# Optimization experiments

Hardware: AMD Instinct MI355X
Metric: run time of the kernel (lower is better)

The kernel has to match this reference:

```python
import jax, jax.numpy as jnp
import numpy as np

FS = 128; WIN = 4; C_IN = 64; C_OUT = 512; BATCH = 1024
K = FS // 4            # conv kernel = 32
STRIDE = K // 2        # 16
WS = FS * WIN          # 512 samples
T = (WS - K) // STRIDE + 1  # 31 time steps
THRESH = 1.0
BN_EPS = 1e-5

# snntorch-style spike with ATan surrogate (alpha=2): fwd Heaviside, bwd 1/(1+(pi*x)^2)
@jax.custom_vjp
def spike_fn(x):
    return (x > 0).astype(x.dtype)

def _spike_fwd(x):
    return (x > 0).astype(x.dtype), x

def _spike_bwd(x, g):
    return (g / (1.0 + (jnp.pi * x) ** 2),)

spike_fn.defvjp(_spike_fwd, _spike_bwd)

def leaky_step(inp, mem, beta):
    # snntorch Leaky, reset_mechanism='subtract': reset computed from PREVIOUS mem, detached
    reset = jax.lax.stop_gradient((mem > THRESH).astype(mem.dtype))
    mem_new = jnp.clip(beta, 0.0, 1.0) * mem + inp - reset * THRESH
    spk = spike_fn(mem_new - THRESH)
    return spk, mem_new

def setup_inputs() -> dict:
    key = jax.random.key(0)
    ks = jax.random.split(key, 10)
    return {
        "x": jax.random.normal(ks[0], (BATCH, C_IN, WS), jnp.float32),
        "conv_w": jax.random.normal(ks[1], (C_OUT, C_IN, K), jnp.float32) * (1.0 / np.sqrt(C_IN * K)),
        "conv_b": jax.random.normal(ks[2], (C_OUT,), jnp.float32) * 0.01,
        "bn_gamma": jnp.ones((C_OUT,), jnp.float32),
        "bn_beta": jnp.zeros((C_OUT,), jnp.float32),
        "bn_mean": jnp.zeros((C_OUT,), jnp.float32),
        "bn_var": jnp.ones((C_OUT,), jnp.float32),
        "fc1_w": jax.random.normal(ks[3], (C_OUT, C_OUT), jnp.float32) * (1.0 / np.sqrt(C_OUT)),
        "fc1_b": jax.random.normal(ks[4], (C_OUT,), jnp.float32) * 0.01,
        "fc2_w": jax.random.normal(ks[5], (2, C_OUT), jnp.float32) * (1.0 / np.sqrt(C_OUT)),
        "fc2_b": jax.random.normal(ks[6], (2,), jnp.float32) * 0.01,
        "beta_enc": jax.random.uniform(ks[7], (C_OUT,), jnp.float32),
        "beta_hid": jax.random.uniform(ks[8], (C_OUT,), jnp.float32),
        "beta_out": jax.random.uniform(ks[9], (2,), jnp.float32),
    }

def reference(x, conv_w, conv_b, bn_gamma, bn_beta, bn_mean, bn_var,
              fc1_w, fc1_b, fc2_w, fc2_b, beta_enc, beta_hid, beta_out):
    # Conv1d: x [B, C_in, WS] -> [B, C_out, T]
    out = jax.lax.conv_general_dilated(
        x, conv_w, window_strides=(STRIDE,), padding='VALID',
        dimension_numbers=('NCH', 'OIH', 'NCH')) + conv_b[None, :, None]
    # BatchNorm1d (eval mode with running stats); dropout is identity in eval
    inv = jax.lax.rsqrt(bn_var + BN_EPS)
    out = bn_gamma[None, :, None] * (out - bn_mean[None, :, None]) * inv[None, :, None] + bn_beta[None, :, None]
    seq = jnp.transpose(out, (2, 0, 1))  # [T, B, C_out]

    mems0 = (jnp.zeros((BATCH, C_OUT), out.dtype),
             jnp.zeros((BATCH, C_OUT), out.dtype),
             jnp.zeros((BATCH, 2), out.dtype))

    def step(carry, xt):
        em, hm, om = carry
        spk_e, em = leaky_step(xt, em, beta_enc)
        cur1 = spk_e @ fc1_w.T + fc1_b
        spk_h, hm = leaky_step(cur1, hm, beta_hid)
        cur2 = spk_h @ fc2_w.T + fc2_b
        spk_o, om = leaky_step(cur2, om, beta_out)
        return (em, hm, om), (spk_o, om)

    (em, hm, om), (spk_rec, mem_rec) = jax.lax.scan(step, mems0, seq)
    return om, spk_rec, mem_rec
```

## Files before the change

kernel.cpp:

```cpp
#include <hip/hip_runtime.h>

#define T_STEPS 31
#define CIN     64
#define COUT    512
#define WSLEN   512
#define CSTRIDE 16
#define KRED    2048
#define NBATCH  1024
#define BCHUNK  512
#define MCHUNK  (BCHUNK * T_STEPS)
#define NMT     (MCHUNK / 16)

typedef int v4i __attribute__((ext_vector_type(4)));

__device__ __forceinline__ double clip01d(double v) { return fmin(fmax(v, 0.0), 1.0); }

__device__ __forceinline__ void gl_lds16(const void* g, void* l) {
    __builtin_amdgcn_global_load_lds(
        (const __attribute__((address_space(1))) void*)g,
        (__attribute__((address_space(3))) void*)l, 16, 0, 0);
}

__device__ __forceinline__ void dig5(float4 f, unsigned int w[5]) {
    float vv[4] = {f.x, f.y, f.z, f.w};
    unsigned int w0 = 0, w1 = 0, w2 = 0, w3 = 0, w4 = 0;
    #pragma unroll
    for (int e = 0; e < 4; ++e) {
        float v  = vv[e];
        float c0 = rintf(v * 16384.0f);
        float r1 = fmaf(c0, -6.103515625e-05f, v);
        float c1 = rintf(r1 * 268435456.0f);
        float r2 = fmaf(c1, -3.725290298461914e-09f, r1);
        float c2 = rintf(r2 * 34359738368.0f);
        int i0 = (int)c0, i1 = (int)c1, i2 = (int)c2;
        int d2 = ((i0 + 64) & 127) - 64;
        int d1 = (i0 - d2) >> 7;
        int d4 = ((i1 + 64) & 127) - 64;
        int d3 = (i1 - d4) >> 7;
        w0 |= (unsigned int)(d1 & 255) << (8 * e);
        w1 |= (unsigned int)(d2 & 255) << (8 * e);
        w2 |= (unsigned int)(d3 & 255) << (8 * e);
        w3 |= (unsigned int)(d4 & 255) << (8 * e);
        w4 |= (unsigned int)(i2 & 255) << (8 * e);
    }
    w[0] = w0; w[1] = w1; w[2] = w2; w[3] = w3; w[4] = w4;
}

__global__ __launch_bounds__(256) void prep_fc1_kernel(
    const float* __restrict__ fc1_w, float* __restrict__ fc1wT)
{
    int idx = blockIdx.x * 256 + threadIdx.x;
    int co = idx & 511;
    int r  = idx >> 9;
    fc1wT[idx] = fc1_w[co * COUT + r];
}

__global__ __launch_bounds__(256) void prep_bd_kernel(
    const float* __restrict__ conv_w, signed char* __restrict__ Bd)
{
    int t  = blockIdx.x * 256 + threadIdx.x;
    int k4 = (t & 511) << 2;
    int co = t >> 9;
    float4 w4 = *(const float4*)(conv_w + (size_t)co * KRED + k4);
    float4 v4 = make_float4(w4.x * 4.0f, w4.y * 4.0f, w4.z * 4.0f, w4.w * 4.0f);
    unsigned int pk[5];
    dig5(v4, pk);
    int off = (((k4 >> 6) * 32 + (co >> 4)) << 10)
            + ((co & 15) + ((k4 >> 4) & 3) * 16) * 16 + (k4 & 15);
    #pragma unroll
    for (int q = 0; q < 5; ++q)
        *(unsigned int*)(Bd + q * 1048576 + off) = pk[q];
}

__global__ __launch_bounds__(256) void prep_fd_kernel(
    const float* __restrict__ fc1_w, signed char* __restrict__ Fd)
{
    int t  = blockIdx.x * 256 + threadIdx.x;
    int k4 = (t & 127) << 2;
    int co = t >> 7;
    float4 w4 = *(const float4*)(fc1_w + (size_t)co * COUT + k4);
    float4 v4 = make_float4(w4.x * 4.0f, w4.y * 4.0f, w4.z * 4.0f, w4.w * 4.0f);
    unsigned int pk[5];
    dig5(v4, pk);
    int off = (((k4 >> 6) * 32 + (co >> 4)) << 10)
            + ((co & 15) + ((k4 >> 4) & 3) * 16) * 16 + (k4 & 15);
    #pragma unroll
    for (int q = 0; q < 5; ++q)
        *(unsigned int*)(Fd + q * 262144 + off) = pk[q];
}

__global__ __launch_bounds__(512) void conv_bn_i8v6_kernel(
    const float* __restrict__ x, const signed char* __restrict__ Bd,
    const float* __restrict__ conv_b,
    const float* __restrict__ bn_gamma, const float* __restrict__ bn_beta,
    const float* __restrict__ bn_mean,  const float* __restrict__ bn_var,
    double* __restrict__ seq, int b_base)
{
    __shared__ __align__(16) signed char Alds[5 * 2048];
    __shared__ __align__(16) signed char Blds[5 * 8192];

    const int tid = threadIdx.x;
    const int nMB = MCHUNK / 32;
    const int bm  = blockIdx.x % nMB;
    const int bnk = blockIdx.x / nMB;
    const int m0 = bm * 32, n0 = bnk * 128;

    const int rA  = tid & 31;
    const int gA  = tid >> 5;
    const int kqA = gA & 3;
    const int jq  = gA >> 2;
    const int mA  = m0 + rA;
    const int bA  = b_base + mA / T_STEPS;
    const int tA  = mA % T_STEPS;
    const float* xp = x + (size_t)bA * CIN * WSLEN + tA * CSTRIDE;
    const int awb  = ((rA >> 4) << 10) + ((rA & 15) + kqA * 16) * 16 + jq * 4;
    const int kloc = kqA * 16 + jq * 4;

    const int wv  = tid >> 6;
    const int l   = tid & 63;
    const int rgM = wv >> 2;
    const int cw  = wv & 3;

    v4i acc[2][5];
    #pragma unroll
    for (int s = 0; s < 2; ++s)
        #pragma unroll
        for (int d = 0; d < 5; ++d) acc[s][d] = (v4i){0, 0, 0, 0};

    float4 sxa = *(const float4*)(xp + (kloc >> 5) * WSLEN + (kloc & 31));

    for (int kt = 0; kt < 32; ++kt) {
        unsigned int pa[5];
        dig5(make_float4(sxa.x * 0.125f, sxa.y * 0.125f, sxa.z * 0.125f, sxa.w * 0.125f), pa);

        __syncthreads();
        #pragma unroll
        for (int p = 0; p < 5; ++p)
            *(unsigned int*)(Alds + p * 2048 + awb) = pa[p];

        #pragma unroll
        for (int i = 0; i < 5; ++i) {
            const int s   = wv * 5 + i;
            const int q   = s >> 3;
            const int ctl = s & 7;
            const signed char* gsrc = Bd + (size_t)q * 1048576
                + (((size_t)(kt * 32 + bnk * 8 + ctl)) << 10) + l * 16;
            gl_lds16(gsrc, Blds + q * 8192 + ctl * 1024);
        }

        if (kt + 1 < 32) {
            int gk = (kt + 1) * 64 + kloc;
            sxa = *(const float4*)(xp + (gk >> 5) * WSLEN + (gk & 31));
        }
        __syncthreads();

        v4i aF[5];
        #pragma unroll
        for (int p = 0; p < 5; ++p)
            aF[p] = *(const v4i*)(Alds + p * 2048 + (rgM << 10) + (l << 4));

        #define MF(A_, B_, C_) __builtin_amdgcn_mfma_i32_16x16x64_i8(A_, B_, C_, 0, 0, 0)
        #pragma unroll
        for (int s = 0; s < 2; ++s) {
            const signed char* bb = Blds + ((cw * 2 + s) << 10) + (l << 4);
            v4i b0 = *(const v4i*)(bb);
            v4i b1 = *(const v4i*)(bb + 8192);
            v4i b2 = *(const v4i*)(bb + 16384);
            v4i b3 = *(const v4i*)(bb + 24576);
            v4i b4 = *(const v4i*)(bb + 32768);
            acc[s][0] = MF(aF[0], b0, acc[s][0]);
            acc[s][1] = MF(aF[1], b0, MF(aF[0], b1, acc[s][1]));
            acc[s][2] = MF(aF[2], b0, MF(aF[1], b1, MF(aF[0], b2, acc[s][2])));
            acc[s][3] = MF(aF[3], b0, MF(aF[2], b1, MF(aF[1], b2, MF(aF[0], b3, acc[s][3]))));
            acc[s][4] = MF(aF[4], b0, MF(aF[3], b1, MF(aF[2], b2, MF(aF[1], b3, MF(aF[0], b4, acc[s][4])))));
        }
        #undef MF
    }

    const int l15 = l & 15;
    const int rq  = l >> 4;
    #pragma unroll
    for (int s = 0; s < 2; ++s) {
        const int co = n0 + (cw * 2 + s) * 16 + l15;
        const double g   = (double)bn_gamma[co];
        const double be  = (double)bn_beta[co];
        const double mn  = (double)bn_mean[co];
        const double vr  = (double)bn_var[co];
        const double cb  = (double)conv_b[co];
        const double inv = 1.0 / sqrt(vr + 1e-5);
        #pragma unroll
        for (int r = 0; r < 4; ++r) {
            double v = (double)acc[s][0][r] * 0x1p-13
                     + (double)acc[s][1][r] * 0x1p-20
                     + (double)acc[s][2][r] * 0x1p-27
                     + (double)acc[s][3][r] * 0x1p-34
                     + (double)acc[s][4][r] * 0x1p-41;
            int m = m0 + rgM * 16 + rq * 4 + r;
            seq[(size_t)m * COUT + co] = g * (v + cb - mn) * inv + be;
        }
    }
}

__global__ __launch_bounds__(512) void enc_scan_kernel(
    const double* __restrict__ seq, const float* __restrict__ beta_enc,
    signed char* __restrict__ Sd)
{
    const int c = threadIdx.x;
    const int b = blockIdx.x;
    const double be = clip01d((double)beta_enc[c]);
    const double* sp = seq + (size_t)b * T_STEPS * COUT + c;
    const size_t cblk = (size_t)(c >> 6) * NMT;
    const int    coff = ((c >> 4) & 3) * 16;
    const int    j    = c & 15;
    double em = 0.0;
    for (int t = 0; t < T_STEPS; ++t) {
        double e = be * em + sp[(size_t)t * COUT] - ((em > 1.0) ? 1.0 : 0.0);
        em = e;
        int m = b * T_STEPS + t;
        Sd[((cblk + (m >> 4)) << 10) + ((m & 15) + coff) * 16 + j] =
            (e > 1.0) ? (signed char)1 : (signed char)0;
    }
}

__global__ __launch_bounds__(512) void fc1_gemm_kernel(
    const signed char* __restrict__ Sd, const signed char* __restrict__ Fd,
    double* __restrict__ cur1)
{
    __shared__ __align__(16) signed char AldsK[2048];
    __shared__ __align__(16) signed char BldsK[5 * 8192];

    const int tid = threadIdx.x;
    const int nMB = MCHUNK / 32;
    const int bm  = blockIdx.x % nMB;
    const int bnk = blockIdx.x / nMB;
    const int m0 = bm * 32, n0 = bnk * 128;

    const int wv  = tid >> 6;
    const int l   = tid & 63;
    const int rgM = wv >> 2;
    const int cw  = wv & 3;

    v4i acc[2][5];
    #pragma unroll
    for (int s = 0; s < 2; ++s)
        #pragma unroll
        for (int d = 0; d < 5; ++d) acc[s][d] = (v4i){0, 0, 0, 0};

    for (int kt = 0; kt < 8; ++kt) {
        __syncthreads();
        #pragma unroll
        for (int i = 0; i < 5; ++i) {
            const int s   = wv * 5 + i;
            const int q   = s >> 3;
            const int ctl = s & 7;
            const signed char* gsrc = Fd + (size_t)q * 262144
                + (((size_t)(kt * 32 + bnk * 8 + ctl)) << 10) + l * 16;
            gl_lds16(gsrc, BldsK + q * 8192 + ctl * 1024);
        }
        if (wv < 2) {
            const signed char* gsrc = Sd
                + (((size_t)(kt * NMT + bm * 2 + wv)) << 10) + l * 16;
            gl_lds16(gsrc, AldsK + wv * 1024);
        }
        __syncthreads();

        v4i aF = *(const v4i*)(AldsK + (rgM << 10) + (l << 4));
        #define MF(A_, B_, C_) __builtin_amdgcn_mfma_i32_16x16x64_i8(A_, B_, C_, 0, 0, 0)
        #pragma unroll
        for (int s = 0; s < 2; ++s) {
            const signed char* bb = BldsK + ((cw * 2 + s) << 10) + (l << 4);
            acc[s][0] = MF(aF, *(const v4i*)(bb),         acc[s][0]);
            acc[s][1] = MF(aF, *(const v4i*)(bb + 8192),  acc[s][1]);
            acc[s][2] = MF(aF, *(const v4i*)(bb + 16384), acc[s][2]);
            acc[s][3] = MF(aF, *(const v4i*)(bb + 24576), acc[s][3]);
            acc[s][4] = MF(aF, *(const v4i*)(bb + 32768), acc[s][4]);
        }
        #undef MF
    }

    const int l15 = l & 15;
    const int rq  = l >> 4;
    #pragma unroll
    for (int s = 0; s < 2; ++s) {
        const int co = n0 + (cw * 2 + s) * 16 + l15;
        #pragma unroll
        for (int r = 0; r < 4; ++r) {
            double v = (double)acc[s][0][r] * 0x1p-9
                     + (double)acc[s][1][r] * 0x1p-16
                     + (double)acc[s][2][r] * 0x1p-23
                     + (double)acc[s][3][r] * 0x1p-30
                     + (double)acc[s][4][r] * 0x1p-37;
            int m = m0 + rgM * 16 + rq * 4 + r;
            cur1[(size_t)m * COUT + co] = v;
        }
    }
}

__global__ __launch_bounds__(512, 4) void hid_out_scan_kernel(
    const double* __restrict__ cur1, const float* __restrict__ fc1_b,
    const float* __restrict__ fc2_w, const float* __restrict__ fc2_b,
    const float* __restrict__ beta_hid, const float* __restrict__ beta_out,
    float* __restrict__ out, int b_base)
{
    __shared__ double red[8][2];

    const int tid  = threadIdx.x;
    const int lane = tid & 63;
    const int wave = tid >> 6;
    const int row  = blockIdx.x;
    const int brow = b_base + row;

    const double bh  = clip01d((double)beta_hid[tid]);
    const double f1b = (double)fc1_b[tid];
    const double w2a = (double)fc2_w[tid];
    const double w2b = (double)fc2_w[COUT + tid];

    double bo = 0.0, f2b = 0.0, om = 0.0;
    if (tid < 2) { bo = clip01d((double)beta_out[tid]); f2b = (double)fc2_b[tid]; }

    double hm = 0.0;
    const double* cp = cur1 + (size_t)row * T_STEPS * COUT + tid;

    for (int t = 0; t < T_STEPS; ++t) {
        double cur = cp[(size_t)t * COUT] + f1b;
        double h = bh * hm + cur - ((hm > 1.0) ? 1.0 : 0.0);
        hm = h;
        double sh = (h > 1.0) ? 1.0 : 0.0;
        double p0 = sh * w2a;
        double p1 = sh * w2b;
        #pragma unroll
        for (int off = 32; off > 0; off >>= 1) {
            p0 += __shfl_down(p0, off);
            p1 += __shfl_down(p1, off);
        }
        if (lane == 0) { red[wave][0] = p0; red[wave][1] = p1; }
        __syncthreads();
        if (tid < 2) {
            double cur2 = f2b;
            #pragma unroll
            for (int w = 0; w < 8; ++w) cur2 += red[w][tid];
            double o = bo * om + cur2 - ((om > 1.0) ? 1.0 : 0.0);
            om = o;
            float so = (o > 1.0) ? 1.0f : 0.0f;
            int bidx = brow * 2 + tid;
            out[2048 + t * 2048 + bidx] = so;
            out[2048 + 63488 + t * 2048 + bidx] = (float)o;
            if (t == T_STEPS - 1) out[bidx] = (float)o;
        }
        __syncthreads();
    }
}

__global__ __launch_bounds__(512, 4) void snn_scan_v3_kernel(
    const double* __restrict__ seq, const float* __restrict__ fc1wT,
    const float* __restrict__ fc1_b, const float* __restrict__ fc2_w,
    const float* __restrict__ fc2_b, const float* __restrict__ beta_enc,
    const float* __restrict__ beta_hid, const float* __restrict__ beta_out,
    float* __restrict__ out, int b_base)
{
    __shared__ int   list[COUT];
    __shared__ int   wcnt[8];
    __shared__ double red[8][2];

    const int tid  = threadIdx.x;
    const int lane = tid & 63;
    const int wave = tid >> 6;
    const int row  = blockIdx.x;
    const int brow = b_base + row;

    const double be  = clip01d((double)beta_enc[tid]);
    const double bh  = clip01d((double)beta_hid[tid]);
    const double f1b = (double)fc1_b[tid];
    const double w2a = (double)fc2_w[tid];
    const double w2b = (double)fc2_w[COUT + tid];

    double bo = 0.0, f2b = 0.0, om = 0.0;
    if (tid < 2) { bo = clip01d((double)beta_out[tid]); f2b = (double)fc2_b[tid]; }

    double em = 0.0, hm = 0.0;
    const double* sp = seq + (size_t)row * T_STEPS * COUT + tid;

    for (int t = 0; t < T_STEPS; ++t) {
        double inp = sp[(size_t)t * COUT];
        double e = be * em + inp - ((em > 1.0) ? 1.0 : 0.0);
        em = e;
        bool spike = (e > 1.0);

        unsigned long long mask = __ballot(spike);
        if (lane == 0) wcnt[wave] = __popcll(mask);
        __syncthreads();

        int base = 0, cnt = 0;
        #pragma unroll
        for (int w = 0; w < 8; ++w) {
            int v = wcnt[w];
            base += (w < wave) ? v : 0;
            cnt  += v;
        }
        if (spike) {
            int pos = base + __popcll(mask & ((1ull << lane) - 1ull));
            list[pos] = tid;
        }
        __syncthreads();

        double s0 = 0.0, s1 = 0.0, s2 = 0.0, s3 = 0.0;
        const float* fw = fc1wT + tid;
        int i = 0;
        for (; i + 4 <= cnt; i += 4) {
            int cA = list[i], cB = list[i + 1], cC = list[i + 2], cD = list[i + 3];
            s0 += (double)fw[(size_t)cA * COUT];
            s1 += (double)fw[(size_t)cB * COUT];
            s2 += (double)fw[(size_t)cC * COUT];
            s3 += (double)fw[(size_t)cD * COUT];
        }
        for (; i < cnt; ++i) s0 += (double)fw[(size_t)list[i] * COUT];
        double cur1 = ((s0 + s1) + (s2 + s3)) + f1b;

        double h = bh * hm + cur1 - ((hm > 1.0) ? 1.0 : 0.0);
        hm = h;
        double sh = (h > 1.0) ? 1.0 : 0.0;
        double p0 = sh * w2a;
        double p1 = sh * w2b;
        #pragma unroll
        for (int off = 32; off > 0; off >>= 1) {
            p0 += __shfl_down(p0, off);
            p1 += __shfl_down(p1, off);
        }
        if (lane == 0) { red[wave][0] = p0; red[wave][1] = p1; }
        __syncthreads();

        if (tid < 2) {
            double cur2 = f2b;
            #pragma unroll
            for (int w = 0; w < 8; ++w) cur2 += red[w][tid];
            double o = bo * om + cur2 - ((om > 1.0) ? 1.0 : 0.0);
            om = o;
            float so = (o > 1.0) ? 1.0f : 0.0f;
            int bidx = brow * 2 + tid;
            out[2048 + t * 2048 + bidx] = so;
            out[2048 + 63488 + t * 2048 + bidx] = (float)o;
            if (t == T_STEPS - 1) out[bidx] = (float)o;
        }
    }
}

extern "C" void kernel_launch(void* const* d_in, const int* in_sizes, int n_in,
                              void* d_out, int out_size, void* d_ws, size_t ws_size,
                              hipStream_t stream)
{
    const float* x        = (const float*)d_in[0];
    const float* conv_w   = (const float*)d_in[1];
    const float* conv_b   = (const float*)d_in[2];
    const float* bn_gamma = (const float*)d_in[3];
    const float* bn_beta  = (const float*)d_in[4];
    const float* bn_mean  = (const float*)d_in[5];
    const float* bn_var   = (const float*)d_in[6];
    const float* fc1_w    = (const float*)d_in[7];
    const float* fc1_b    = (const float*)d_in[8];
    const float* fc2_w    = (const float*)d_in[9];
    const float* fc2_b    = (const float*)d_in[10];
    const float* beta_enc = (const float*)d_in[11];
    const float* beta_hid = (const float*)d_in[12];
    const float* beta_out = (const float*)d_in[13];
    float* out = (float*)d_out;

    const size_t NEED_BIG = 16ull * 1048576 + (size_t)MCHUNK * COUT * 8;
    signed char* Bd = (signed char*)d_ws;

    if (ws_size >= NEED_BIG) {
        signed char* Fd  = (signed char*)d_ws + 5 * 1048576;
        signed char* Sd  = (signed char*)d_ws + 7 * 1048576;
        double*      seq = (double*)((char*)d_ws + 16 * 1048576);

        prep_bd_kernel<<<1024, 256, 0, stream>>>(conv_w, Bd);
        prep_fd_kernel<<<256, 256, 0, stream>>>(fc1_w, Fd);

        for (int chunk = 0; chunk < 2; ++chunk) {
            int b_base = chunk * BCHUNK;
            conv_bn_i8v6_kernel<<<(MCHUNK / 32) * (COUT / 128), 512, 0, stream>>>(
                x, Bd, conv_b, bn_gamma, bn_beta, bn_mean, bn_var, seq, b_base);
            enc_scan_kernel<<<BCHUNK, 512, 0, stream>>>(seq, beta_enc, Sd);
            fc1_gemm_kernel<<<(MCHUNK / 32) * (COUT / 128), 512, 0, stream>>>(
                Sd, Fd, seq);
            hid_out_scan_kernel<<<BCHUNK, 512, 0, stream>>>(
                seq, fc1_b, fc2_w, fc2_b, beta_hid, beta_out, out, b_base);
        }
    } else {
        float*  fc1wT = (float*)((char*)d_ws + 5 * 1048576);
        double* seq   = (double*)((char*)d_ws + 6 * 1048576);

        prep_bd_kernel<<<1024, 256, 0, stream>>>(conv_w, Bd);
        prep_fc1_kernel<<<1024, 256, 0, stream>>>(fc1_w, fc1wT);

        for (int chunk = 0; chunk < 2; ++chunk) {
            int b_base = chunk * BCHUNK;
            conv_bn_i8v6_kernel<<<(MCHUNK / 32) * (COUT / 128), 512, 0, stream>>>(
                x, Bd, conv_b, bn_gamma, bn_beta, bn_mean, bn_var, seq, b_base);
            snn_scan_v3_kernel<<<BCHUNK, 512, 0, stream>>>(
                seq, fc1wT, fc1_b, fc2_w, fc2_b, beta_enc, beta_hid, beta_out, out, b_base);
        }
    }
}
```

Before: 712.4 us.

## Double-buffer conv GEMM LDS tiles and halve N tile per block

The conv+BN int8 MFMA kernel now double-buffers its A and B tiles in LDS. The next k-step's global-to-LDS loads and input digit splitting overlap the current step's MFMAs, so the loop needs one barrier per iteration instead of two. The N tile per block shrinks from 128 to 64 output channels, which doubles the grid size and halves per-wave accumulators. In exchange, each block has fewer MFMAs per barrier and the conv weights are loaded twice as often overall.

```diff
diff --git a/kernel.cpp b/kernel.cpp
--- a/kernel.cpp
+++ b/kernel.cpp
@@ -89,21 +89,21 @@
         *(unsigned int*)(Fd + q * 262144 + off) = pk[q];
 }
 
-__global__ __launch_bounds__(512) void conv_bn_i8v6_kernel(
+__global__ __launch_bounds__(512) void conv_bn_i8v8_kernel(
     const float* __restrict__ x, const signed char* __restrict__ Bd,
     const float* __restrict__ conv_b,
     const float* __restrict__ bn_gamma, const float* __restrict__ bn_beta,
     const float* __restrict__ bn_mean,  const float* __restrict__ bn_var,
     double* __restrict__ seq, int b_base)
 {
-    __shared__ __align__(16) signed char Alds[5 * 2048];
-    __shared__ __align__(16) signed char Blds[5 * 8192];
+    __shared__ __align__(16) signed char Abuf[2][5 * 2048];
+    __shared__ __align__(16) signed char Bbuf[2][5 * 4096];
 
     const int tid = threadIdx.x;
     const int nMB = MCHUNK / 32;
     const int bm  = blockIdx.x % nMB;
     const int bnk = blockIdx.x / nMB;
-    const int m0 = bm * 32, n0 = bnk * 128;
+    const int m0 = bm * 32, n0 = bnk * 64;
 
     const int rA  = tid & 31;
     const int gA  = tid >> 5;
@@ -119,69 +119,91 @@
     const int wv  = tid >> 6;
     const int l   = tid & 63;
     const int rgM = wv >> 2;
-    const int cw  = wv & 3;
-
-    v4i acc[2][5];
+    const int cwv = wv & 3;
+
+    v4i acc[5];
     #pragma unroll
-    for (int s = 0; s < 2; ++s)
-        #pragma unroll
-        for (int d = 0; d < 5; ++d) acc[s][d] = (v4i){0, 0, 0, 0};
+    for (int d = 0; d < 5; ++d) acc[d] = (v4i){0, 0, 0, 0};
 
     float4 sxa = *(const float4*)(xp + (kloc >> 5) * WSLEN + (kloc & 31));
+    {
+        unsigned int pa[5];
+        dig5(make_float4(sxa.x * 0.125f, sxa.y * 0.125f,
+                         sxa.z * 0.125f, sxa.w * 0.125f), pa);
+        #pragma unroll
+        for (int p = 0; p < 5; ++p)
+            *(unsigned int*)(&Abuf[0][p * 2048 + awb]) = pa[p];
+        #pragma unroll
+        for (int i = 0; i < 3; ++i) {
+            int s = wv + 8 * i;
+            if (s < 20) {
+                int q = s >> 2, ctl = s & 3;
+                const signed char* gsrc = Bd + (size_t)q * 1048576
+                    + (((size_t)(bnk * 4 + ctl)) << 10) + l * 16;
+                gl_lds16(gsrc, &Bbuf[0][q * 4096 + ctl * 1024]);
+            }
+        }
+        int gk = 64 + kloc;
+        sxa = *(const float4*)(xp + (gk >> 5) * WSLEN + (gk & 31));
+    }
+    __syncthreads();
 
     for (int kt = 0; kt < 32; ++kt) {
+        const int cur = kt & 1, nxt = cur ^ 1;
+        const bool more = (kt + 1 < 32);
+
+        if (more) {
+            #pragma unroll
+            for (int i = 0; i < 3; ++i) {
+                int s = wv + 8 * i;
+                if (s < 20) {
+                    int q = s >> 2, ctl = s & 3;
+                    const signed char* gsrc = Bd + (size_t)q * 1048576
+                        + (((size_t)((kt + 1) * 32 + bnk * 4 + ctl)) << 10) + l * 16;
+                    gl_lds16(gsrc, &Bbuf[nxt][q * 4096 + ctl * 1024]);
+                }
+            }
+        }
+
         unsigned int pa[5];
-        dig5(make_float4(sxa.x * 0.125f, sxa.y * 0.125f, sxa.z * 0.125f, sxa.w * 0.125f), pa);
-
-        __syncthreads();
+        if (more)
+            dig5(make_float4(sxa.x * 0.125f, sxa.y * 0.125f,
+                             sxa.z * 0.125f, sxa.w * 0.125f), pa);
+
+        if (kt + 2 < 32) {
+            int gk = (kt + 2) * 64 + kloc;
+            sxa = *(const float4*)(xp + (gk >> 5) * WSLEN + (gk & 31));
+        }
+
+        v4i aF[5], bF[5];
         #pragma unroll
         for (int p = 0; p < 5; ++p)
-            *(unsigned int*)(Alds + p * 2048 + awb) = pa[p];
-
-        #pragma unroll
-        for (int i = 0; i < 5; ++i) {
-            const int s   = wv * 5 + i;
-            const int q   = s >> 3;
-            const int ctl = s & 7;
-            const signed char* gsrc = Bd + (size_t)q * 1048576
-                + (((size_t)(kt * 32 + bnk * 8 + ctl)) << 10) + l * 16;
-            gl_lds16(gsrc, Blds + q * 8192 + ctl * 1024);
-        }
-
-        if (kt + 1 < 32) {
-            int gk = (kt + 1) * 64 + kloc;
-            sxa = *(const float4*)(xp + (gk >> 5) * WSLEN + (gk & 31));
-        }
-        __syncthreads();
-
-        v4i aF[5];
-        #pragma unroll
-        for (int p = 0; p < 5; ++p)
-            aF[p] = *(const v4i*)(Alds + p * 2048 + (rgM << 10) + (l << 4));
+            aF[p] = *(const v4i*)(&Abuf[cur][p * 2048 + (rgM << 10) + (l << 4)]);
+        #pragma unroll
+        for (int q = 0; q < 5; ++q)
+            bF[q] = *(const v4i*)(&Bbuf[cur][q * 4096 + (cwv << 10) + (l << 4)]);
 
         #define MF(A_, B_, C_) __builtin_amdgcn_mfma_i32_16x16x64_i8(A_, B_, C_, 0, 0, 0)
-        #pragma unroll
-        for (int s = 0; s < 2; ++s) {
-            const signed char* bb = Blds + ((cw * 2 + s) << 10) + (l << 4);
-            v4i b0 = *(const v4i*)(bb);
-            v4i b1 = *(const v4i*)(bb + 8192);
-            v4i b2 = *(const v4i*)(bb + 16384);
-            v4i b3 = *(const v4i*)(bb + 24576);
-            v4i b4 = *(const v4i*)(bb + 32768);
-            acc[s][0] = MF(aF[0], b0, acc[s][0]);
-            acc[s][1] = MF(aF[1], b0, MF(aF[0], b1, acc[s][1]));
-            acc[s][2] = MF(aF[2], b0, MF(aF[1], b1, MF(aF[0], b2, acc[s][2])));
-            acc[s][3] = MF(aF[3], b0, MF(aF[2], b1, MF(aF[1], b2, MF(aF[0], b3, acc[s][3]))));
-            acc[s][4] = MF(aF[4], b0, MF(aF[3], b1, MF(aF[2], b2, MF(aF[1], b3, MF(aF[0], b4, acc[s][4])))));
-        }
+        acc[0] = MF(aF[0], bF[0], acc[0]);
+        acc[1] = MF(aF[1], bF[0], MF(aF[0], bF[1], acc[1]));
+        acc[2] = MF(aF[2], bF[0], MF(aF[1], bF[1], MF(aF[0], bF[2], acc[2])));
+        acc[3] = MF(aF[3], bF[0], MF(aF[2], bF[1], MF(aF[1], bF[2], MF(aF[0], bF[3], acc[3]))));
+        acc[4] = MF(aF[4], bF[0], MF(aF[3], bF[1], MF(aF[2], bF[2], MF(aF[1], bF[3], MF(aF[0], bF[4], acc[4])))));
         #undef MF
+
+        if (more) {
+            #pragma unroll
+            for (int p = 0; p < 5; ++p)
+                *(unsigned int*)(&Abuf[nxt][p * 2048 + awb]) = pa[p];
+        }
+
+        __syncthreads();
     }
 
     const int l15 = l & 15;
     const int rq  = l >> 4;
-    #pragma unroll
-    for (int s = 0; s < 2; ++s) {
-        const int co = n0 + (cw * 2 + s) * 16 + l15;
+    {
+        const int co = n0 + cwv * 16 + l15;
         const double g   = (double)bn_gamma[co];
         const double be  = (double)bn_beta[co];
         const double mn  = (double)bn_mean[co];
@@ -190,11 +212,11 @@
         const double inv = 1.0 / sqrt(vr + 1e-5);
         #pragma unroll
         for (int r = 0; r < 4; ++r) {
-            double v = (double)acc[s][0][r] * 0x1p-13
-                     + (double)acc[s][1][r] * 0x1p-20
-                     + (double)acc[s][2][r] * 0x1p-27
-                     + (double)acc[s][3][r] * 0x1p-34
-                     + (double)acc[s][4][r] * 0x1p-41;
+            double v = (double)acc[0][r] * 0x1p-13
+                     + (double)acc[1][r] * 0x1p-20
+                     + (double)acc[2][r] * 0x1p-27
+                     + (double)acc[3][r] * 0x1p-34
+                     + (double)acc[4][r] * 0x1p-41;
             int m = m0 + rgM * 16 + rq * 4 + r;
             seq[(size_t)m * COUT + co] = g * (v + cb - mn) * inv + be;
         }
@@ -477,7 +499,7 @@
 
         for (int chunk = 0; chunk < 2; ++chunk) {
             int b_base = chunk * BCHUNK;
-            conv_bn_i8v6_kernel<<<(MCHUNK / 32) * (COUT / 128), 512, 0, stream>>>(
+            conv_bn_i8v8_kernel<<<(MCHUNK / 32) * (COUT / 64), 512, 0, stream>>>(
                 x, Bd, conv_b, bn_gamma, bn_beta, bn_mean, bn_var, seq, b_base);
             enc_scan_kernel<<<BCHUNK, 512, 0, stream>>>(seq, beta_enc, Sd);
             fc1_gemm_kernel<<<(MCHUNK / 32) * (COUT / 128), 512, 0, stream>>>(
@@ -494,7 +516,7 @@
 
         for (int chunk = 0; chunk < 2; ++chunk) {
             int b_base = chunk * BCHUNK;
-            conv_bn_i8v6_kernel<<<(MCHUNK / 32) * (COUT / 128), 512, 0, stream>>>(
+            conv_bn_i8v8_kernel<<<(MCHUNK / 32) * (COUT / 64), 512, 0, stream>>>(
                 x, Bd, conv_b, bn_gamma, bn_beta, bn_mean, bn_var, seq, b_base);
             snn_scan_v3_kernel<<<BCHUNK, 512, 0, stream>>>(
                 seq, fc1wT, fc1_b, fc2_w, fc2_b, beta_enc, beta_hid, beta_out, out, b_base);
```

Result: slower. 866.6 us (+21.6%).

## Fuse encoder LIF scan into conv GEMM epilogue, one batch row per block

Applied to the files above, without the earlier changes.

The conv GEMM now tiles M as one batch row per block: 31 time steps, padded to 32 by duplicating t=30. The BN output is staged in shared memory, and 128 threads run the encoder leaky scan directly, writing int8 spikes. This removes the separate enc_scan kernel and the write and read of the large double seq buffer. It also drops the small-workspace fallback path. In exchange the block does one redundant row of MFMA work, and the serial scan runs on only 128 threads at the end of each block.

```diff
diff --git a/kernel.cpp b/kernel.cpp
--- a/kernel.cpp
+++ b/kernel.cpp
@@ -46,15 +46,6 @@
     w[0] = w0; w[1] = w1; w[2] = w2; w[3] = w3; w[4] = w4;
 }
 
-__global__ __launch_bounds__(256) void prep_fc1_kernel(
-    const float* __restrict__ fc1_w, float* __restrict__ fc1wT)
-{
-    int idx = blockIdx.x * 256 + threadIdx.x;
-    int co = idx & 511;
-    int r  = idx >> 9;
-    fc1wT[idx] = fc1_w[co * COUT + r];
-}
-
 __global__ __launch_bounds__(256) void prep_bd_kernel(
     const float* __restrict__ conv_w, signed char* __restrict__ Bd)
 {
@@ -89,29 +80,29 @@
         *(unsigned int*)(Fd + q * 262144 + off) = pk[q];
 }
 
-__global__ __launch_bounds__(512) void conv_bn_i8v6_kernel(
+__global__ __launch_bounds__(512) void conv_enc_kernel(
     const float* __restrict__ x, const signed char* __restrict__ Bd,
     const float* __restrict__ conv_b,
     const float* __restrict__ bn_gamma, const float* __restrict__ bn_beta,
     const float* __restrict__ bn_mean,  const float* __restrict__ bn_var,
-    double* __restrict__ seq, int b_base)
-{
-    __shared__ __align__(16) signed char Alds[5 * 2048];
-    __shared__ __align__(16) signed char Blds[5 * 8192];
+    const float* __restrict__ beta_enc, signed char* __restrict__ Sd,
+    int b_base)
+{
+    __shared__ __align__(16) signed char smem[51200];
+    signed char* Alds = smem;
+    signed char* Blds = smem + 10240;
 
     const int tid = threadIdx.x;
-    const int nMB = MCHUNK / 32;
-    const int bm  = blockIdx.x % nMB;
-    const int bnk = blockIdx.x / nMB;
-    const int m0 = bm * 32, n0 = bnk * 128;
+    const int bm  = blockIdx.x & 511;
+    const int bnk = blockIdx.x >> 9;
+    const int n0  = bnk * 128;
 
     const int rA  = tid & 31;
     const int gA  = tid >> 5;
     const int kqA = gA & 3;
     const int jq  = gA >> 2;
-    const int mA  = m0 + rA;
-    const int bA  = b_base + mA / T_STEPS;
-    const int tA  = mA % T_STEPS;
+    const int bA  = b_base + bm;
+    const int tA  = (rA == 31) ? 30 : rA;
     const float* xp = x + (size_t)bA * CIN * WSLEN + tA * CSTRIDE;
     const int awb  = ((rA >> 4) << 10) + ((rA & 15) + kqA * 16) * 16 + jq * 4;
     const int kloc = kqA * 16 + jq * 4;
@@ -131,7 +122,8 @@
 
     for (int kt = 0; kt < 32; ++kt) {
         unsigned int pa[5];
-        dig5(make_float4(sxa.x * 0.125f, sxa.y * 0.125f, sxa.z * 0.125f, sxa.w * 0.125f), pa);
+        dig5(make_float4(sxa.x * 0.125f, sxa.y * 0.125f,
+                         sxa.z * 0.125f, sxa.w * 0.125f), pa);
 
         __syncthreads();
         #pragma unroll
@@ -177,11 +169,14 @@
         #undef MF
     }
 
+    __syncthreads();
+    double* st = (double*)smem;
     const int l15 = l & 15;
     const int rq  = l >> 4;
     #pragma unroll
     for (int s = 0; s < 2; ++s) {
-        const int co = n0 + (cw * 2 + s) * 16 + l15;
+        const int cl = (cw * 2 + s) * 16 + l15;
+        const int co = n0 + cl;
         const double g   = (double)bn_gamma[co];
         const double be  = (double)bn_beta[co];
         const double mn  = (double)bn_mean[co];
@@ -195,30 +190,27 @@
                      + (double)acc[s][2][r] * 0x1p-27
                      + (double)acc[s][3][r] * 0x1p-34
                      + (double)acc[s][4][r] * 0x1p-41;
-            int m = m0 + rgM * 16 + rq * 4 + r;
-            seq[(size_t)m * COUT + co] = g * (v + cb - mn) * inv + be;
-        }
-    }
-}
-
-__global__ __launch_bounds__(512) void enc_scan_kernel(
-    const double* __restrict__ seq, const float* __restrict__ beta_enc,
-    signed char* __restrict__ Sd)
-{
-    const int c = threadIdx.x;
-    const int b = blockIdx.x;
-    const double be = clip01d((double)beta_enc[c]);
-    const double* sp = seq + (size_t)b * T_STEPS * COUT + c;
-    const size_t cblk = (size_t)(c >> 6) * NMT;
-    const int    coff = ((c >> 4) & 3) * 16;
-    const int    j    = c & 15;
-    double em = 0.0;
-    for (int t = 0; t < T_STEPS; ++t) {
-        double e = be * em + sp[(size_t)t * COUT] - ((em > 1.0) ? 1.0 : 0.0);
-        em = e;
-        int m = b * T_STEPS + t;
-        Sd[((cblk + (m >> 4)) << 10) + ((m & 15) + coff) * 16 + j] =
-            (e > 1.0) ? (signed char)1 : (signed char)0;
+            int t = rgM * 16 + rq * 4 + r;
+            st[t * 128 + cl] = g * (v + cb - mn) * inv + be;
+        }
+    }
+    __syncthreads();
+
+    if (tid < 128) {
+        const int cl = tid;
+        const int co = n0 + cl;
+        const double bee = clip01d((double)beta_enc[co]);
+        const size_t cblk = (size_t)(co >> 6) * NMT;
+        const int coff = ((co >> 4) & 3) * 16;
+        const int j    = co & 15;
+        double em = 0.0;
+        for (int t = 0; t < T_STEPS; ++t) {
+            double e = bee * em + st[t * 128 + cl] - ((em > 1.0) ? 1.0 : 0.0);
+            em = e;
+            int m = bm * T_STEPS + t;
+            Sd[((cblk + (m >> 4)) << 10) + ((m & 15) + coff) * 16 + j] =
+                (e > 1.0) ? (signed char)1 : (signed char)0;
+        }
     }
 }
 
@@ -348,99 +340,6 @@
             if (t == T_STEPS - 1) out[bidx] = (float)o;
         }
         __syncthreads();
-    }
-}
-
-__global__ __launch_bounds__(512, 4) void snn_scan_v3_kernel(
-    const double* __restrict__ seq, const float* __restrict__ fc1wT,
-    const float* __restrict__ fc1_b, const float* __restrict__ fc2_w,
-    const float* __restrict__ fc2_b, const float* __restrict__ beta_enc,
-    const float* __restrict__ beta_hid, const float* __restrict__ beta_out,
-    float* __restrict__ out, int b_base)
-{
-    __shared__ int   list[COUT];
-    __shared__ int   wcnt[8];
-    __shared__ double red[8][2];
-
-    const int tid  = threadIdx.x;
-    const int lane = tid & 63;
-    const int wave = tid >> 6;
-    const int row  = blockIdx.x;
-    const int brow = b_base + row;
-
-    const double be  = clip01d((double)beta_enc[tid]);
-    const double bh  = clip01d((double)beta_hid[tid]);
-    const double f1b = (double)fc1_b[tid];
-    const double w2a = (double)fc2_w[tid];
-    const double w2b = (double)fc2_w[COUT + tid];
-
-    double bo = 0.0, f2b = 0.0, om = 0.0;
-    if (tid < 2) { bo = clip01d((double)beta_out[tid]); f2b = (double)fc2_b[tid]; }
-
-    double em = 0.0, hm = 0.0;
-    const double* sp = seq + (size_t)row * T_STEPS * COUT + tid;
-
-    for (int t = 0; t < T_STEPS; ++t) {
-        double inp = sp[(size_t)t * COUT];
-        double e = be * em + inp - ((em > 1.0) ? 1.0 : 0.0);
-        em = e;
-        bool spike = (e > 1.0);
-
-        unsigned long long mask = __ballot(spike);
-        if (lane == 0) wcnt[wave] = __popcll(mask);
-        __syncthreads();
-
-        int base = 0, cnt = 0;
-        #pragma unroll
-        for (int w = 0; w < 8; ++w) {
-            int v = wcnt[w];
-            base += (w < wave) ? v : 0;
-            cnt  += v;
-        }
-        if (spike) {
-            int pos = base + __popcll(mask & ((1ull << lane) - 1ull));
-            list[pos] = tid;
-        }
-        __syncthreads();
-
-        double s0 = 0.0, s1 = 0.0, s2 = 0.0, s3 = 0.0;
-        const float* fw = fc1wT + tid;
-        int i = 0;
-        for (; i + 4 <= cnt; i += 4) {
-            int cA = list[i], cB = list[i + 1], cC = list[i + 2], cD = list[i + 3];
-            s0 += (double)fw[(size_t)cA * COUT];
-            s1 += (double)fw[(size_t)cB * COUT];
-            s2 += (double)fw[(size_t)cC * COUT];
-            s3 += (double)fw[(size_t)cD * COUT];
-        }
-        for (; i < cnt; ++i) s0 += (double)fw[(size_t)list[i] * COUT];
-        double cur1 = ((s0 + s1) + (s2 + s3)) + f1b;
-
-        double h = bh * hm + cur1 - ((hm > 1.0) ? 1.0 : 0.0);
-        hm = h;
-        double sh = (h > 1.0) ? 1.0 : 0.0;
-        double p0 = sh * w2a;
-        double p1 = sh * w2b;
-        #pragma unroll
-        for (int off = 32; off > 0; off >>= 1) {
-            p0 += __shfl_down(p0, off);
-            p1 += __shfl_down(p1, off);
-        }
-        if (lane == 0) { red[wave][0] = p0; red[wave][1] = p1; }
-        __syncthreads();
-
-        if (tid < 2) {
-            double cur2 = f2b;
-            #pragma unroll
-            for (int w = 0; w < 8; ++w) cur2 += red[w][tid];
-            double o = bo * om + cur2 - ((om > 1.0) ? 1.0 : 0.0);
-            om = o;
-            float so = (o > 1.0) ? 1.0f : 0.0f;
-            int bidx = brow * 2 + tid;
-            out[2048 + t * 2048 + bidx] = so;
-            out[2048 + 63488 + t * 2048 + bidx] = (float)o;
-            if (t == T_STEPS - 1) out[bidx] = (float)o;
-        }
     }
 }
 
@@ -464,40 +363,22 @@
     const float* beta_out = (const float*)d_in[13];
     float* out = (float*)d_out;
 
-    const size_t NEED_BIG = 16ull * 1048576 + (size_t)MCHUNK * COUT * 8;
-    signed char* Bd = (signed char*)d_ws;
-
-    if (ws_size >= NEED_BIG) {
-        signed char* Fd  = (signed char*)d_ws + 5 * 1048576;
-        signed char* Sd  = (signed char*)d_ws + 7 * 1048576;
-        double*      seq = (double*)((char*)d_ws + 16 * 1048576);
-
-        prep_bd_kernel<<<1024, 256, 0, stream>>>(conv_w, Bd);
-        prep_fd_kernel<<<256, 256, 0, stream>>>(fc1_w, Fd);
-
-        for (int chunk = 0; chunk < 2; ++chunk) {
-            int b_base = chunk * BCHUNK;
-            conv_bn_i8v6_kernel<<<(MCHUNK / 32) * (COUT / 128), 512, 0, stream>>>(
-                x, Bd, conv_b, bn_gamma, bn_beta, bn_mean, bn_var, seq, b_base);
-            enc_scan_kernel<<<BCHUNK, 512, 0, stream>>>(seq, beta_enc, Sd);
-            fc1_gemm_kernel<<<(MCHUNK / 32) * (COUT / 128), 512, 0, stream>>>(
-                Sd, Fd, seq);
-            hid_out_scan_kernel<<<BCHUNK, 512, 0, stream>>>(
-                seq, fc1_b, fc2_w, fc2_b, beta_hid, beta_out, out, b_base);
-        }
-    } else {
-        float*  fc1wT = (float*)((char*)d_ws + 5 * 1048576);
-        double* seq   = (double*)((char*)d_ws + 6 * 1048576);
-
-        prep_bd_kernel<<<1024, 256, 0, stream>>>(conv_w, Bd);
-        prep_fc1_kernel<<<1024, 256, 0, stream>>>(fc1_w, fc1wT);
-
-        for (int chunk = 0; chunk < 2; ++chunk) {
-            int b_base = chunk * BCHUNK;
-            conv_bn_i8v6_kernel<<<(MCHUNK / 32) * (COUT / 128), 512, 0, stream>>>(
-                x, Bd, conv_b, bn_gamma, bn_beta, bn_mean, bn_var, seq, b_base);
-            snn_scan_v3_kernel<<<BCHUNK, 512, 0, stream>>>(
-                seq, fc1wT, fc1_b, fc2_w, fc2_b, beta_enc, beta_hid, beta_out, out, b_base);
-        }
-    }
-}
+    signed char* Bd   = (signed char*)d_ws;
+    signed char* Fd   = (signed char*)d_ws + 5 * 1048576;
+    signed char* Sd   = (signed char*)d_ws + 7 * 1048576;
+    double*      cur1 = (double*)((char*)d_ws + 16 * 1048576);
+
+    prep_bd_kernel<<<1024, 256, 0, stream>>>(conv_w, Bd);
+    prep_fd_kernel<<<256, 256, 0, stream>>>(fc1_w, Fd);
+
+    for (int chunk = 0; chunk < 2; ++chunk) {
+        int b_base = chunk * BCHUNK;
+        conv_enc_kernel<<<BCHUNK * (COUT / 128), 512, 0, stream>>>(
+            x, Bd, conv_b, bn_gamma, bn_beta, bn_mean, bn_var,
+            beta_enc, Sd, b_base);
+        fc1_gemm_kernel<<<(MCHUNK / 32) * (COUT / 128), 512, 0, stream>>>(
+            Sd, Fd, cur1);
+        hid_out_scan_kernel<<<BCHUNK, 512, 0, stream>>>(
+            cur1, fc1_b, fc2_w, fc2_b, beta_hid, beta_out, out, b_base);
+    }
+}
```

Result: slower. 968.9 us (+36.0%).
